# Kernel optimization log

Measured on AMD Instinct MI355X. Metric: run time of the kernel, lower is better.

The kernel has to match this reference:

```python
import jax, jax.numpy as jnp
import numpy as np

D_MODEL = 512; D_INNER = 1024; D_SSM = 512; D_STATE = 16; DT_RANK = 32; D_CONV = 4
BETA = 0.0; ALPHA = 1.0  # module defaults: no momentum -> vanilla Longhorn scan
B = 8; L = 2048


def dwconv_silu(x, w, b):
    # x: (B, C, L), w: (C, 1, K); torch F.conv1d(padding='same') with K=4 pads (left=1, right=2)
    y = jax.lax.conv_general_dilated(
        x, w, window_strides=(1,), padding=[(1, 2)],
        dimension_numbers=('NCH', 'OIH', 'NCH'), feature_group_count=x.shape[1])
    y = y + b[None, :, None]
    return y * jax.nn.sigmoid(y)


def longhorn_scan(u, q, k, dt, D_skip, t_bias):
    # u, dt: (B, D, L); q, k: (B, N, L). Longhorn online-learner SSM with momentum velocity.
    delta = jax.nn.softplus(dt + t_bias[None, :, None])           # (B, D, L)
    k2 = jnp.sum(k * k, axis=1, keepdims=True)                    # (B, 1, L)
    eps = delta / (1.0 + delta * k2)                              # implicit-update step size

    def step(carry, inp):
        S, v = carry                                              # (B, D, N) each
        eps_t, u_t, k_t, q_t = inp                                # (B,D),(B,D),(B,N),(B,N)
        g = eps_t[:, :, None] * (u_t[:, :, None] - S * k_t[:, None, :]) * k_t[:, None, :]
        v = BETA * v + ALPHA * g                                  # momentum velocity
        S = S + v
        y_t = jnp.einsum('bdn,bn->bd', S, q_t)
        return (S, v), y_t

    Bq, Dm, _ = u.shape
    S0 = jnp.zeros((Bq, Dm, q.shape[1]), u.dtype)
    xs = (jnp.moveaxis(eps, 2, 0), jnp.moveaxis(u, 2, 0),
          jnp.moveaxis(k, 2, 0), jnp.moveaxis(q, 2, 0))
    _, ys = jax.lax.scan(step, (S0, S0), xs)                      # ys: (L, B, D)
    return jnp.moveaxis(ys, 0, 2) + D_skip[None, :, None] * u    # (B, D, L)


def setup_inputs() -> dict:
    key = jax.random.key(0)
    ks = jax.random.split(key, 12)
    s = lambda k, shape, sc: jax.random.normal(k, shape, jnp.float32) * sc
    dt0 = jnp.exp(jax.random.uniform(ks[8], (D_SSM,), jnp.float32,
                                     float(np.log(1e-3)), float(np.log(1e-1))))
    b_dt = jnp.log(jnp.expm1(dt0))  # inv-softplus init as in torch module
    return {
        'hidden_states': s(ks[0], (B, L, D_MODEL), 1.0),
        'W_in': s(ks[1], (D_INNER, D_MODEL), 0.02),
        'conv_x_w': s(ks[2], (D_SSM, 1, D_CONV), 0.3),
        'conv_x_b': s(ks[3], (D_SSM,), 0.02),
        'conv_z_w': s(ks[4], (D_SSM, 1, D_CONV), 0.3),
        'conv_z_b': s(ks[5], (D_SSM,), 0.02),
        'W_xproj': s(ks[6], (DT_RANK + 2 * D_STATE, D_SSM), 0.05),
        'W_dt': s(ks[7], (D_SSM, DT_RANK), DT_RANK ** -0.5),
        'b_dt': b_dt,
        'D_skip': jnp.ones((D_SSM,), jnp.float32),
        'W_out': s(ks[9], (D_MODEL, D_INNER), 0.02),
    }


def reference(hidden_states, W_in, conv_x_w, conv_x_b, conv_z_w, conv_z_b,
              W_xproj, W_dt, b_dt, D_skip, W_out):
    xz = jnp.einsum('bld,ed->ble', hidden_states, W_in)           # (B, L, d_inner)
    xz = jnp.swapaxes(xz, 1, 2)                                   # (B, d_inner, L)
    x, z = xz[:, :D_SSM], xz[:, D_SSM:]
    x = dwconv_silu(x, conv_x_w, conv_x_b)
    z = dwconv_silu(z, conv_z_w, conv_z_b)
    x_dbl = jnp.einsum('bdl,ed->bel', x, W_xproj)                 # (B, r+2N, L)
    dt_low = x_dbl[:, :DT_RANK]
    k = x_dbl[:, DT_RANK:DT_RANK + D_STATE]
    q = x_dbl[:, DT_RANK + D_STATE:]
    dt = jnp.einsum('dr,brl->bdl', W_dt, dt_low)                  # (B, d_ssm, L)
    y = longhorn_scan(x, q, k, dt, D_skip, b_dt)                  # (B, d_ssm, L)
    y = jnp.concatenate([y, z], axis=1)                           # (B, d_inner, L)
    y = jnp.swapaxes(y, 1, 2)                                     # (B, L, d_inner)
    return jnp.einsum('ble,de->bld', y, W_out)                    # (B, L, d_model)
```

## Files before the change

kernel.cpp:

```cpp
#include <hip/hip_runtime.h>
#include <hip/hip_bf16.h>
#include <math.h>

#define BB 8
#define LL 2048
#define DMODEL 512
#define DINNER 1024
#define DSSM 512
#define NST 16
#define DTR 32
#define CCH 64
#define LC (LL / CCH)
#define BDN (BB * DSSM * NST)
#define CLW 8

typedef short short8 __attribute__((ext_vector_type(8)));
typedef float f32x4 __attribute__((ext_vector_type(4)));

__device__ __forceinline__ unsigned short f2bf(float f) {
  unsigned u = __float_as_uint(f);
  u += 0x7FFFu + ((u >> 16) & 1u);
  return (unsigned short)(u >> 16);
}
__device__ __forceinline__ float bf2f(unsigned short s) {
  return __uint_as_float(((unsigned)s) << 16);
}

__device__ __forceinline__ void gload16(const void* g, void* l) {
  __builtin_amdgcn_global_load_lds(
      (const __attribute__((address_space(1))) void*)g,
      (__attribute__((address_space(3))) void*)l, 16, 0, 0);
}

template<bool OUTBF>
__global__ __launch_bounds__(256) void gemm_bf16(
    const unsigned short* __restrict__ Ab,
    const unsigned short* __restrict__ Wb,
    void* __restrict__ Cout, int K, int NBN) {
  __shared__ unsigned short tA[128 * 64];
  __shared__ unsigned short tW[128 * 64];
  const int tid = threadIdx.x;
  const int ln = tid & 63;
  const int wv = tid >> 6;
  const int wr = wv >> 1, wc = wv & 1;
  const int lr = ln & 15, kc = ln >> 4;

  const int nwg = gridDim.x;
  const int q = nwg >> 3;
  const int bid = blockIdx.x;
  const int wg = (bid & 7) * q + (bid >> 3);
  const int mblk = wg / NBN, nblk = wg % NBN;
  const size_t m0 = (size_t)mblk * 128, n0 = (size_t)nblk * 128;

  f32x4 acc[4][4];
#pragma unroll
  for (int m = 0; m < 4; ++m)
#pragma unroll
    for (int n = 0; n < 4; ++n)
#pragma unroll
      for (int j = 0; j < 4; ++j) acc[m][n][j] = 0.f;

  const int wbase = (tid & 0xC0) << 4;

  for (int k0 = 0; k0 < K; k0 += 64) {
#pragma unroll
    for (int it = 0; it < 4; ++it) {
      const int gi = it * 256 + tid;
      const int r = gi >> 3, s = gi & 7, g = s ^ (r & 7);
      const size_t off = (m0 + r) * (size_t)K + (size_t)(k0 + g * 8);
      gload16(Ab + off, (char*)tA + it * 4096 + wbase);
    }
#pragma unroll
    for (int it = 0; it < 4; ++it) {
      const int gi = it * 256 + tid;
      const int r = gi >> 3, s = gi & 7, g = s ^ (r & 7);
      const size_t off = (n0 + r) * (size_t)K + (size_t)(k0 + g * 8);
      gload16(Wb + off, (char*)tW + it * 4096 + wbase);
    }
    __syncthreads();

    short8 alo[4], ahi[4], wlo[4], whi[4];
#pragma unroll
    for (int m = 0; m < 4; ++m) {
      const int ra = wr * 64 + m * 16 + lr;
      const int sl = kc ^ (ra & 7);
      const char* base = (const char*)tA + ra * 128;
      alo[m] = *(const short8*)(base + sl * 16);
      ahi[m] = *(const short8*)(base + (sl ^ 4) * 16);
    }
#pragma unroll
    for (int n = 0; n < 4; ++n) {
      const int rb = wc * 64 + n * 16 + lr;
      const int sl = kc ^ (rb & 7);
      const char* base = (const char*)tW + rb * 128;
      wlo[n] = *(const short8*)(base + sl * 16);
      whi[n] = *(const short8*)(base + (sl ^ 4) * 16);
    }
#pragma unroll
    for (int m = 0; m < 4; ++m)
#pragma unroll
      for (int n = 0; n < 4; ++n) {
        acc[m][n] = __builtin_amdgcn_mfma_f32_16x16x32_bf16(alo[m], wlo[n], acc[m][n], 0, 0, 0);
        acc[m][n] = __builtin_amdgcn_mfma_f32_16x16x32_bf16(ahi[m], whi[n], acc[m][n], 0, 0, 0);
      }
    __syncthreads();
  }

  const int ldc = NBN * 128;
#pragma unroll
  for (int m = 0; m < 4; ++m) {
    const size_t row0 = m0 + wr * 64 + m * 16 + kc * 4;
#pragma unroll
    for (int n = 0; n < 4; ++n) {
      const size_t col = n0 + wc * 64 + n * 16 + lr;
#pragma unroll
      for (int j = 0; j < 4; ++j) {
        if (OUTBF)
          ((unsigned short*)Cout)[(row0 + j) * (size_t)ldc + col] = f2bf(acc[m][n][j]);
        else
          ((float*)Cout)[(row0 + j) * (size_t)ldc + col] = acc[m][n][j];
      }
    }
  }
}

__global__ __launch_bounds__(256) void cvt_kernel(const float* __restrict__ in,
    unsigned short* __restrict__ o, int n4) {
  int i = blockIdx.x * 256 + threadIdx.x;
  const int str = gridDim.x * 256;
  for (; i < n4; i += str) {
    const float4 v = ((const float4*)in)[i];
    ushort4 h;
    h.x = f2bf(v.x); h.y = f2bf(v.y); h.z = f2bf(v.z); h.w = f2bf(v.w);
    ((ushort4*)o)[i] = h;
  }
}

__global__ __launch_bounds__(256) void gemm_xproj(
    const float* __restrict__ A, const float* __restrict__ W,
    float* __restrict__ C) {
  __shared__ float As[32][16];
  __shared__ float Ws[32][64];
  const int t = threadIdx.x;
  const int tn = t & 63, tm = t >> 6;
  const size_t m0 = (size_t)blockIdx.x * 16;
  float acc[4] = {0.f, 0.f, 0.f, 0.f};

  for (int k0 = 0; k0 < 512; k0 += 32) {
    if (t < 128) {
      const int r = t >> 3, c4 = (t & 7) << 2;
      const float4 v = *(const float4*)(A + (m0 + r) * 512 + k0 + c4);
      As[c4 + 0][r] = v.x; As[c4 + 1][r] = v.y;
      As[c4 + 2][r] = v.z; As[c4 + 3][r] = v.w;
    }
#pragma unroll
    for (int rep = 0; rep < 2; rep++) {
      const int f = t + rep * 256;
      const int n = f >> 3, c4 = (f & 7) << 2;
      const float4 v = *(const float4*)(W + n * 512 + k0 + c4);
      Ws[c4 + 0][n] = v.x; Ws[c4 + 1][n] = v.y;
      Ws[c4 + 2][n] = v.z; Ws[c4 + 3][n] = v.w;
    }
    __syncthreads();
#pragma unroll
    for (int k = 0; k < 32; k++) {
      const float4 a4 = *(const float4*)&As[k][tm * 4];
      const float w = Ws[k][tn];
      acc[0] = fmaf(a4.x, w, acc[0]);
      acc[1] = fmaf(a4.y, w, acc[1]);
      acc[2] = fmaf(a4.z, w, acc[2]);
      acc[3] = fmaf(a4.w, w, acc[3]);
    }
    __syncthreads();
  }
#pragma unroll
  for (int i = 0; i < 4; i++)
    C[(m0 + tm * 4 + i) * 64 + tn] = acc[i];
}

__global__ __launch_bounds__(256) void conv_silu_kernel(
    const unsigned short* __restrict__ xzB,
    const float* __restrict__ cxw, const float* __restrict__ cxb,
    const float* __restrict__ czw, const float* __restrict__ czb,
    float* __restrict__ xc, unsigned short* __restrict__ yB) {
  const int c = blockIdx.x * 256 + threadIdx.x;
  const int l0 = blockIdx.y * CLW;
  const int b = blockIdx.z;
  float w0, w1, w2, w3, bias;
  if (c < DSSM) {
    w0 = cxw[c * 4 + 0]; w1 = cxw[c * 4 + 1]; w2 = cxw[c * 4 + 2]; w3 = cxw[c * 4 + 3];
    bias = cxb[c];
  } else {
    const int cz = c - DSSM;
    w0 = czw[cz * 4 + 0]; w1 = czw[cz * 4 + 1]; w2 = czw[cz * 4 + 2]; w3 = czw[cz * 4 + 3];
    bias = czb[cz];
  }
  const unsigned short* base = xzB + ((size_t)b * LL + l0) * DINNER + c;
  float v[CLW + 3];
  v[0] = (l0 > 0) ? bf2f(base[-(int)DINNER]) : 0.f;
#pragma unroll
  for (int i = 0; i <= CLW + 1; i++) {
    const int l = l0 + i;
    v[i + 1] = (l < LL) ? bf2f(base[(size_t)i * DINNER]) : 0.f;
  }
#pragma unroll
  for (int j = 0; j < CLW; j++) {
    float a = bias;
    a = fmaf(v[j + 0], w0, a);
    a = fmaf(v[j + 1], w1, a);
    a = fmaf(v[j + 2], w2, a);
    a = fmaf(v[j + 3], w3, a);
    const float y = a / (1.f + expf(-a));
    const size_t bl = (size_t)b * LL + l0 + j;
    if (c < DSSM)
      xc[bl * DSSM + c] = y;
    else
      yB[bl * DINNER + c] = f2bf(y);
  }
}

__global__ __launch_bounds__(256) void dteps_kernel(
    const float* __restrict__ xdbl, const float* __restrict__ W_dt,
    const float* __restrict__ b_dt, float* __restrict__ eps) {
  __shared__ float sW[512 * 36];
  __shared__ float sd[16 * 64];
  __shared__ float sk2[16];
  const int t = threadIdx.x;
  const size_t bl0 = (size_t)blockIdx.x * 16;

#pragma unroll
  for (int it = 0; it < 16; it++) {
    const int i = it * 256 + t;
    const int d = i >> 3, j = i & 7;
    const float4 v = ((const float4*)W_dt)[i];
    *(float4*)&sW[d * 36 + j * 4] = v;
  }
  {
    const float4 v = ((const float4*)(xdbl + bl0 * 64))[t];
    *(float4*)&sd[t * 4] = v;
  }
  __syncthreads();
  {
    const int il = t >> 4, n = t & 15;
    float v = sd[il * 64 + 32 + n];
    v *= v;
    v += __shfl_xor(v, 1); v += __shfl_xor(v, 2);
    v += __shfl_xor(v, 4); v += __shfl_xor(v, 8);
    if (n == 0) sk2[il] = v;
  }
  const int d0 = t, d1 = t + 256;
  float W0[32], W1[32];
#pragma unroll
  for (int j4 = 0; j4 < 8; j4++) {
    *(float4*)&W0[j4 * 4] = *(const float4*)&sW[d0 * 36 + j4 * 4];
    *(float4*)&W1[j4 * 4] = *(const float4*)&sW[d1 * 36 + j4 * 4];
  }
  const float b0 = b_dt[d0], b1 = b_dt[d1];
  __syncthreads();

#pragma unroll
  for (int il = 0; il < 16; il++) {
    float dl[32];
#pragma unroll
    for (int j4 = 0; j4 < 8; j4++)
      *(float4*)&dl[j4 * 4] = *(const float4*)&sd[il * 64 + j4 * 4];
    const float k2 = sk2[il];
    float dt0 = b0, dt1 = b1;
#pragma unroll
    for (int r = 0; r < 32; r++) {
      dt0 = fmaf(W0[r], dl[r], dt0);
      dt1 = fmaf(W1[r], dl[r], dt1);
    }
    const float del0 = (dt0 > 20.f) ? dt0 : log1pf(expf(dt0));
    const float del1 = (dt1 > 20.f) ? dt1 : log1pf(expf(dt1));
    const size_t row = (bl0 + il) * DSSM;
    eps[row + d0] = del0 / (1.f + del0 * k2);
    eps[row + d1] = del1 / (1.f + del1 * k2);
  }
}

__global__ __launch_bounds__(256) void scan_passA(
    const float* __restrict__ eps, const float* __restrict__ xc,
    const float* __restrict__ xdbl,
    float* __restrict__ Ach, float* __restrict__ Bch) {
  const int d = blockIdx.x * 256 + threadIdx.x;
  const int b = blockIdx.y, ch = blockIdx.z;
  const size_t bl0 = (size_t)b * LL + (size_t)ch * LC;
  const float* ep = eps + bl0 * DSSM + d;
  const float* up = xc + bl0 * DSSM + d;
  const float* kq = xdbl + bl0 * 64;
  float A[16], S[16];
#pragma unroll
  for (int n = 0; n < 16; n++) { A[n] = 1.f; S[n] = 0.f; }
#pragma unroll 2
  for (int j = 0; j < LC; j++) {
    const float e = ep[(size_t)j * DSSM];
    const float u = up[(size_t)j * DSSM];
    const float* kj = kq + j * 64 + 32;
#pragma unroll
    for (int n = 0; n < 16; n++) {
      const float k = kj[n];
      const float t0 = e * k;
      const float a = fmaf(-t0, k, 1.f);
      A[n] *= a;
      S[n] = fmaf(S[n], a, t0 * u);
    }
  }
  const size_t base = (size_t)ch * BDN + (((size_t)b * DSSM + d) << 4);
#pragma unroll
  for (int n4 = 0; n4 < 4; n4++) {
    ((float4*)(Ach + base))[n4] =
        make_float4(A[4 * n4], A[4 * n4 + 1], A[4 * n4 + 2], A[4 * n4 + 3]);
    ((float4*)(Bch + base))[n4] =
        make_float4(S[4 * n4], S[4 * n4 + 1], S[4 * n4 + 2], S[4 * n4 + 3]);
  }
}

__global__ __launch_bounds__(256) void scan_passB(
    const float* __restrict__ Ach, const float* __restrict__ Bch,
    float* __restrict__ S0) {
  const size_t i = (size_t)blockIdx.x * 256 + threadIdx.x;
  float S = 0.f;
  for (int ch = 0; ch < CCH; ch++) {
    const size_t off = (size_t)ch * BDN + i;
    const float a = Ach[off];
    const float bv = Bch[off];
    S0[off] = S;
    S = fmaf(S, a, bv);
  }
}

__global__ __launch_bounds__(256) void scan_passC(
    const float* __restrict__ eps, const float* __restrict__ xc,
    const float* __restrict__ xdbl, const float* __restrict__ D_skip,
    const float* __restrict__ S0, unsigned short* __restrict__ yB) {
  const int d = blockIdx.x * 256 + threadIdx.x;
  const int b = blockIdx.y, ch = blockIdx.z;
  const size_t bl0 = (size_t)b * LL + (size_t)ch * LC;
  const float* ep = eps + bl0 * DSSM + d;
  const float* up = xc + bl0 * DSSM + d;
  const float* kq = xdbl + bl0 * 64;
  unsigned short* yp = yB + bl0 * DINNER + d;
  const float Dv = D_skip[d];
  const size_t base = (size_t)ch * BDN + (((size_t)b * DSSM + d) << 4);
  float S[16];
#pragma unroll
  for (int n4 = 0; n4 < 4; n4++) {
    const float4 v = ((const float4*)(S0 + base))[n4];
    S[4 * n4 + 0] = v.x; S[4 * n4 + 1] = v.y;
    S[4 * n4 + 2] = v.z; S[4 * n4 + 3] = v.w;
  }
#pragma unroll 2
  for (int j = 0; j < LC; j++) {
    const float e = ep[(size_t)j * DSSM];
    const float u = up[(size_t)j * DSSM];
    const float* kj = kq + j * 64 + 32;
#pragma unroll
    for (int n = 0; n < 16; n++) {
      const float k = kj[n];
      const float t0 = e * k;
      const float a = fmaf(-t0, k, 1.f);
      S[n] = fmaf(S[n], a, t0 * u);
    }
    float y0 = 0.f, y1 = 0.f, y2 = 0.f, y3 = 0.f;
#pragma unroll
    for (int n = 0; n < 16; n += 4) {
      y0 = fmaf(S[n + 0], kj[16 + n + 0], y0);
      y1 = fmaf(S[n + 1], kj[16 + n + 1], y1);
      y2 = fmaf(S[n + 2], kj[16 + n + 2], y2);
      y3 = fmaf(S[n + 3], kj[16 + n + 3], y3);
    }
    const float yv = fmaf(Dv, u, (y0 + y1) + (y2 + y3));
    yp[(size_t)j * DINNER] = f2bf(yv);
  }
}

extern "C" void kernel_launch(void* const* d_in, const int* in_sizes, int n_in,
                              void* d_out, int out_size, void* d_ws, size_t ws_size,
                              hipStream_t stream) {
  const float* hidden  = (const float*)d_in[0];
  const float* W_in    = (const float*)d_in[1];
  const float* cxw     = (const float*)d_in[2];
  const float* cxb     = (const float*)d_in[3];
  const float* czw     = (const float*)d_in[4];
  const float* czb     = (const float*)d_in[5];
  const float* W_xproj = (const float*)d_in[6];
  const float* W_dt    = (const float*)d_in[7];
  const float* b_dt    = (const float*)d_in[8];
  const float* D_skip  = (const float*)d_in[9];
  const float* W_out   = (const float*)d_in[10];
  float* out = (float*)d_out;

  const size_t ML  = (size_t)BB * LL;
  const size_t MK5 = ML * DSSM;
  const size_t MN  = ML * DINNER;
  const size_t WIN = (size_t)DINNER * DMODEL;
  const size_t WOU = (size_t)DMODEL * DINNER;
  const size_t CB  = (size_t)CCH * BDN;

  unsigned short* hidB  = (unsigned short*)d_ws;
  unsigned short* WinB  = hidB + MK5;
  unsigned short* WoutB = WinB + WIN;
  unsigned short* xzB   = WoutB + WOU;
  unsigned short* yB    = xzB + MN;
  float* xc   = (float*)(yB + MN);
  float* xdbl = xc + MK5;
  float* eps  = xdbl + ML * 64;
  float* Ach  = eps + MK5;
  float* Bch  = Ach + CB;
  float* S0   = Bch + CB;

  cvt_kernel<<<2048, 256, 0, stream>>>(hidden, hidB, (int)(MK5 / 4));
  cvt_kernel<<<512, 256, 0, stream>>>(W_in, WinB, (int)(WIN / 4));
  cvt_kernel<<<512, 256, 0, stream>>>(W_out, WoutB, (int)(WOU / 4));

  gemm_bf16<true><<<(16384 / 128) * (1024 / 128), 256, 0, stream>>>(
      hidB, WinB, xzB, DMODEL, DINNER / 128);

  conv_silu_kernel<<<dim3(DINNER / 256, LL / CLW, BB), 256, 0, stream>>>(
      xzB, cxw, cxb, czw, czb, xc, yB);

  gemm_xproj<<<dim3(1024), 256, 0, stream>>>(xc, W_xproj, xdbl);

  dteps_kernel<<<dim3(1024), 256, 0, stream>>>(xdbl, W_dt, b_dt, eps);

  scan_passA<<<dim3(2, BB, CCH), 256, 0, stream>>>(eps, xc, xdbl, Ach, Bch);
  scan_passB<<<dim3(BDN / 256), 256, 0, stream>>>(Ach, Bch, S0);
  scan_passC<<<dim3(2, BB, CCH), 256, 0, stream>>>(
      eps, xc, xdbl, D_skip, S0, yB);

  gemm_bf16<false><<<(16384 / 128) * (512 / 128), 256, 0, stream>>>(
      yB, WoutB, out, DINNER, DMODEL / 128);
}
```

Before: 326.1 us.

## Fold W_dt into x-projection weights and run fused projection on bf16 MFMA GEMM

Precomputes W_dt·W_xproj[:32] and concatenates it with the k/q projection rows into one 640x512 bf16 weight. The separate fp32 x-proj GEMM and the dt low-rank GEMM are replaced by a single tensor-core GEMM writing dt, k and q directly. The conv output x is now stored as bf16, which halves its traffic in the scans. A simpler elementwise eps kernel follows, and the workspace is reorganised to alias the scan buffers over dead ones. This costs a larger GEMM output (640 columns instead of 64) and lower precision for x and dt.

```diff
diff --git a/kernel.cpp b/kernel.cpp
--- a/kernel.cpp
+++ b/kernel.cpp
@@ -9,6 +9,7 @@
 #define DSSM 512
 #define NST 16
 #define DTR 32
+#define NXD 640
 #define CCH 64
 #define LC (LL / CCH)
 #define BDN (BB * DSSM * NST)
@@ -136,53 +137,31 @@
   }
 }
 
-__global__ __launch_bounds__(256) void gemm_xproj(
-    const float* __restrict__ A, const float* __restrict__ W,
-    float* __restrict__ C) {
-  __shared__ float As[32][16];
-  __shared__ float Ws[32][64];
-  const int t = threadIdx.x;
-  const int tn = t & 63, tm = t >> 6;
-  const size_t m0 = (size_t)blockIdx.x * 16;
-  float acc[4] = {0.f, 0.f, 0.f, 0.f};
-
-  for (int k0 = 0; k0 < 512; k0 += 32) {
-    if (t < 128) {
-      const int r = t >> 3, c4 = (t & 7) << 2;
-      const float4 v = *(const float4*)(A + (m0 + r) * 512 + k0 + c4);
-      As[c4 + 0][r] = v.x; As[c4 + 1][r] = v.y;
-      As[c4 + 2][r] = v.z; As[c4 + 3][r] = v.w;
-    }
-#pragma unroll
-    for (int rep = 0; rep < 2; rep++) {
-      const int f = t + rep * 256;
-      const int n = f >> 3, c4 = (f & 7) << 2;
-      const float4 v = *(const float4*)(W + n * 512 + k0 + c4);
-      Ws[c4 + 0][n] = v.x; Ws[c4 + 1][n] = v.y;
-      Ws[c4 + 2][n] = v.z; Ws[c4 + 3][n] = v.w;
-    }
-    __syncthreads();
-#pragma unroll
-    for (int k = 0; k < 32; k++) {
-      const float4 a4 = *(const float4*)&As[k][tm * 4];
-      const float w = Ws[k][tn];
-      acc[0] = fmaf(a4.x, w, acc[0]);
-      acc[1] = fmaf(a4.y, w, acc[1]);
-      acc[2] = fmaf(a4.z, w, acc[2]);
-      acc[3] = fmaf(a4.w, w, acc[3]);
-    }
-    __syncthreads();
-  }
-#pragma unroll
-  for (int i = 0; i < 4; i++)
-    C[(m0 + tm * 4 + i) * 64 + tn] = acc[i];
+__global__ __launch_bounds__(256) void weff_kernel(
+    const float* __restrict__ W_dt, const float* __restrict__ W_xproj,
+    unsigned short* __restrict__ WcatB) {
+  const int c = blockIdx.x * 256 + threadIdx.x;
+  const int r0 = blockIdx.y;
+  float v;
+  if (r0 < 512) {
+    float acc = 0.f;
+#pragma unroll
+    for (int r = 0; r < 32; r++)
+      acc = fmaf(W_dt[r0 * 32 + r], W_xproj[r * 512 + c], acc);
+    v = acc;
+  } else if (r0 < 544) {
+    v = W_xproj[(r0 - 480) * 512 + c];
+  } else {
+    v = 0.f;
+  }
+  WcatB[(size_t)r0 * 512 + c] = f2bf(v);
 }
 
 __global__ __launch_bounds__(256) void conv_silu_kernel(
     const unsigned short* __restrict__ xzB,
     const float* __restrict__ cxw, const float* __restrict__ cxb,
     const float* __restrict__ czw, const float* __restrict__ czb,
-    float* __restrict__ xc, unsigned short* __restrict__ yB) {
+    unsigned short* __restrict__ xcB, unsigned short* __restrict__ yB) {
   const int c = blockIdx.x * 256 + threadIdx.x;
   const int l0 = blockIdx.y * CLW;
   const int b = blockIdx.z;
@@ -213,90 +192,45 @@
     const float y = a / (1.f + expf(-a));
     const size_t bl = (size_t)b * LL + l0 + j;
     if (c < DSSM)
-      xc[bl * DSSM + c] = y;
+      xcB[bl * DSSM + c] = f2bf(y);
     else
       yB[bl * DINNER + c] = f2bf(y);
   }
 }
 
-__global__ __launch_bounds__(256) void dteps_kernel(
-    const float* __restrict__ xdbl, const float* __restrict__ W_dt,
-    const float* __restrict__ b_dt, float* __restrict__ eps) {
-  __shared__ float sW[512 * 36];
-  __shared__ float sd[16 * 64];
-  __shared__ float sk2[16];
-  const int t = threadIdx.x;
-  const size_t bl0 = (size_t)blockIdx.x * 16;
-
-#pragma unroll
-  for (int it = 0; it < 16; it++) {
-    const int i = it * 256 + t;
-    const int d = i >> 3, j = i & 7;
-    const float4 v = ((const float4*)W_dt)[i];
-    *(float4*)&sW[d * 36 + j * 4] = v;
-  }
-  {
-    const float4 v = ((const float4*)(xdbl + bl0 * 64))[t];
-    *(float4*)&sd[t * 4] = v;
-  }
-  __syncthreads();
-  {
-    const int il = t >> 4, n = t & 15;
-    float v = sd[il * 64 + 32 + n];
-    v *= v;
-    v += __shfl_xor(v, 1); v += __shfl_xor(v, 2);
-    v += __shfl_xor(v, 4); v += __shfl_xor(v, 8);
-    if (n == 0) sk2[il] = v;
-  }
-  const int d0 = t, d1 = t + 256;
-  float W0[32], W1[32];
-#pragma unroll
-  for (int j4 = 0; j4 < 8; j4++) {
-    *(float4*)&W0[j4 * 4] = *(const float4*)&sW[d0 * 36 + j4 * 4];
-    *(float4*)&W1[j4 * 4] = *(const float4*)&sW[d1 * 36 + j4 * 4];
-  }
-  const float b0 = b_dt[d0], b1 = b_dt[d1];
-  __syncthreads();
-
-#pragma unroll
-  for (int il = 0; il < 16; il++) {
-    float dl[32];
-#pragma unroll
-    for (int j4 = 0; j4 < 8; j4++)
-      *(float4*)&dl[j4 * 4] = *(const float4*)&sd[il * 64 + j4 * 4];
-    const float k2 = sk2[il];
-    float dt0 = b0, dt1 = b1;
-#pragma unroll
-    for (int r = 0; r < 32; r++) {
-      dt0 = fmaf(W0[r], dl[r], dt0);
-      dt1 = fmaf(W1[r], dl[r], dt1);
-    }
-    const float del0 = (dt0 > 20.f) ? dt0 : log1pf(expf(dt0));
-    const float del1 = (dt1 > 20.f) ? dt1 : log1pf(expf(dt1));
-    const size_t row = (bl0 + il) * DSSM;
-    eps[row + d0] = del0 / (1.f + del0 * k2);
-    eps[row + d1] = del1 / (1.f + del1 * k2);
-  }
+__global__ __launch_bounds__(256) void dteps2_kernel(
+    const float* __restrict__ xdbl2, const float* __restrict__ b_dt,
+    float* __restrict__ eps) {
+  const int half = blockIdx.x;
+  const size_t row = blockIdx.y;
+  const int d = half * 256 + threadIdx.x;
+  const float* rp = xdbl2 + row * NXD;
+  float k2 = 0.f;
+#pragma unroll
+  for (int n = 0; n < 16; n++) { const float kv = rp[512 + n]; k2 = fmaf(kv, kv, k2); }
+  const float dt = rp[d] + b_dt[d];
+  const float delta = (dt > 20.f) ? dt : log1pf(expf(dt));
+  eps[row * DSSM + d] = delta / (1.f + delta * k2);
 }
 
 __global__ __launch_bounds__(256) void scan_passA(
-    const float* __restrict__ eps, const float* __restrict__ xc,
-    const float* __restrict__ xdbl,
+    const float* __restrict__ eps, const unsigned short* __restrict__ xcB,
+    const float* __restrict__ xdbl2,
     float* __restrict__ Ach, float* __restrict__ Bch) {
   const int d = blockIdx.x * 256 + threadIdx.x;
   const int b = blockIdx.y, ch = blockIdx.z;
   const size_t bl0 = (size_t)b * LL + (size_t)ch * LC;
   const float* ep = eps + bl0 * DSSM + d;
-  const float* up = xc + bl0 * DSSM + d;
-  const float* kq = xdbl + bl0 * 64;
+  const unsigned short* up = xcB + bl0 * DSSM + d;
+  const float* kq = xdbl2 + bl0 * NXD + 512;
   float A[16], S[16];
 #pragma unroll
   for (int n = 0; n < 16; n++) { A[n] = 1.f; S[n] = 0.f; }
 #pragma unroll 2
   for (int j = 0; j < LC; j++) {
     const float e = ep[(size_t)j * DSSM];
-    const float u = up[(size_t)j * DSSM];
-    const float* kj = kq + j * 64 + 32;
+    const float u = bf2f(up[(size_t)j * DSSM]);
+    const float* kj = kq + j * NXD;
 #pragma unroll
     for (int n = 0; n < 16; n++) {
       const float k = kj[n];
@@ -331,15 +265,15 @@
 }
 
 __global__ __launch_bounds__(256) void scan_passC(
-    const float* __restrict__ eps, const float* __restrict__ xc,
-    const float* __restrict__ xdbl, const float* __restrict__ D_skip,
+    const float* __restrict__ eps, const unsigned short* __restrict__ xcB,
+    const float* __restrict__ xdbl2, const float* __restrict__ D_skip,
     const float* __restrict__ S0, unsigned short* __restrict__ yB) {
   const int d = blockIdx.x * 256 + threadIdx.x;
   const int b = blockIdx.y, ch = blockIdx.z;
   const size_t bl0 = (size_t)b * LL + (size_t)ch * LC;
   const float* ep = eps + bl0 * DSSM + d;
-  const float* up = xc + bl0 * DSSM + d;
-  const float* kq = xdbl + bl0 * 64;
+  const unsigned short* up = xcB + bl0 * DSSM + d;
+  const float* kq = xdbl2 + bl0 * NXD + 512;
   unsigned short* yp = yB + bl0 * DINNER + d;
   const float Dv = D_skip[d];
   const size_t base = (size_t)ch * BDN + (((size_t)b * DSSM + d) << 4);
@@ -353,8 +287,8 @@
 #pragma unroll 2
   for (int j = 0; j < LC; j++) {
     const float e = ep[(size_t)j * DSSM];
-    const float u = up[(size_t)j * DSSM];
-    const float* kj = kq + j * 64 + 32;
+    const float u = bf2f(up[(size_t)j * DSSM]);
+    const float* kj = kq + j * NXD;
 #pragma unroll
     for (int n = 0; n < 16; n++) {
       const float k = kj[n];
@@ -396,38 +330,42 @@
   const size_t MN  = ML * DINNER;
   const size_t WIN = (size_t)DINNER * DMODEL;
   const size_t WOU = (size_t)DMODEL * DINNER;
+  const size_t WCT = (size_t)NXD * DMODEL;
   const size_t CB  = (size_t)CCH * BDN;
 
-  unsigned short* hidB  = (unsigned short*)d_ws;
-  unsigned short* WinB  = hidB + MK5;
+  unsigned short* WinB  = (unsigned short*)d_ws;
   unsigned short* WoutB = WinB + WIN;
-  unsigned short* xzB   = WoutB + WOU;
-  unsigned short* yB    = xzB + MN;
-  float* xc   = (float*)(yB + MN);
-  float* xdbl = xc + MK5;
-  float* eps  = xdbl + ML * 64;
-  float* Ach  = eps + MK5;
-  float* Bch  = Ach + CB;
-  float* S0   = Bch + CB;
+  unsigned short* WcatB = WoutB + WOU;
+  unsigned short* xcB   = WcatB + WCT;
+  unsigned short* yB    = xcB + MK5;
+  float* xdbl2 = (float*)(yB + MN);
+  float* eps   = xdbl2 + ML * NXD;
+  unsigned short* hidB = (unsigned short*)(eps + MK5);
+  unsigned short* xzB  = hidB + MK5;
+  float* Ach = (float*)hidB;
+  float* Bch = Ach + CB;
+  float* S0  = Bch + CB;
 
   cvt_kernel<<<2048, 256, 0, stream>>>(hidden, hidB, (int)(MK5 / 4));
   cvt_kernel<<<512, 256, 0, stream>>>(W_in, WinB, (int)(WIN / 4));
   cvt_kernel<<<512, 256, 0, stream>>>(W_out, WoutB, (int)(WOU / 4));
+  weff_kernel<<<dim3(2, NXD), 256, 0, stream>>>(W_dt, W_xproj, WcatB);
 
   gemm_bf16<true><<<(16384 / 128) * (1024 / 128), 256, 0, stream>>>(
       hidB, WinB, xzB, DMODEL, DINNER / 128);
 
   conv_silu_kernel<<<dim3(DINNER / 256, LL / CLW, BB), 256, 0, stream>>>(
-      xzB, cxw, cxb, czw, czb, xc, yB);
-
-  gemm_xproj<<<dim3(1024), 256, 0, stream>>>(xc, W_xproj, xdbl);
-
-  dteps_kernel<<<dim3(1024), 256, 0, stream>>>(xdbl, W_dt, b_dt, eps);
-
-  scan_passA<<<dim3(2, BB, CCH), 256, 0, stream>>>(eps, xc, xdbl, Ach, Bch);
+      xzB, cxw, cxb, czw, czb, xcB, yB);
+
+  gemm_bf16<false><<<(16384 / 128) * (NXD / 128), 256, 0, stream>>>(
+      xcB, WcatB, xdbl2, DMODEL, NXD / 128);
+
+  dteps2_kernel<<<dim3(2, (unsigned)ML), 256, 0, stream>>>(xdbl2, b_dt, eps);
+
+  scan_passA<<<dim3(2, BB, CCH), 256, 0, stream>>>(eps, xcB, xdbl2, Ach, Bch);
   scan_passB<<<dim3(BDN / 256), 256, 0, stream>>>(Ach, Bch, S0);
   scan_passC<<<dim3(2, BB, CCH), 256, 0, stream>>>(
-      eps, xc, xdbl, D_skip, S0, yB);
+      eps, xcB, xdbl2, D_skip, S0, yB);
 
   gemm_bf16<false><<<(16384 / 128) * (512 / 128), 256, 0, stream>>>(
       yB, WoutB, out, DINNER, DMODEL / 128);
```

Measured after the change: 286.8 us. 12.1% less time.
